# Kernel optimization log

Measured on AMD Instinct MI355X. Metric: run time of the kernel, lower is better.

Reference implementation:

```python
import jax, jax.numpy as jnp
import numpy as np

NUM_HEADS = 16


def setup_inputs() -> dict:
    key = jax.random.key(0)
    k1, k2, k3 = jax.random.split(key, 3)
    B, S, C = 1, 4096, 1024
    x = jax.random.normal(k1, (B, S, C), dtype=jnp.float32)
    # additive causal mask: 0 on/below diagonal, -1e9 above
    causal = jnp.triu(jnp.full((S, S), -1e9, dtype=jnp.float32), k=1)
    attention_mask = causal[None, None, :, :]
    W_attn = jax.random.normal(k2, (C, 3 * C), dtype=jnp.float32) * (C ** -0.5)
    b_attn = jnp.zeros((3 * C,), dtype=jnp.float32)
    W_proj = jax.random.normal(k3, (C, C), dtype=jnp.float32) * (C ** -0.5)
    b_proj = jnp.zeros((C,), dtype=jnp.float32)
    return {"x": x, "attention_mask": attention_mask, "W_attn": W_attn,
            "b_attn": b_attn, "W_proj": W_proj, "b_proj": b_proj}


def reference(x, attention_mask, W_attn, b_attn, W_proj, b_proj):
    B, S, C = x.shape
    H = NUM_HEADS
    hd = C // H
    qkv = x @ W_attn + b_attn                      # [B,S,3C]
    q, k, v = jnp.split(qkv, 3, axis=-1)
    # [B,S,C] -> [B,H,S,hd]
    q = q.reshape(B, S, H, hd).transpose(0, 2, 1, 3)
    k = k.reshape(B, S, H, hd).transpose(0, 2, 1, 3)
    v = v.reshape(B, S, H, hd).transpose(0, 2, 1, 3)
    att = jnp.einsum('bhqd,bhkd->bhqk', q, k) / jnp.sqrt(jnp.float32(hd))
    att = att + attention_mask                     # additive causal mask
    att = jax.nn.softmax(att, axis=-1)             # dropout is identity (p=0/eval)
    out = jnp.einsum('bhqk,bhkd->bhqd', att, v)    # [B,H,S,hd]
    out = out.transpose(0, 2, 1, 3).reshape(B, S, C)
    return out @ W_proj + b_proj
```

## Files before the change

kernel.cpp:

```cpp
#include <hip/hip_runtime.h>
#include <stdint.h>


typedef __bf16 bf16x8 __attribute__((ext_vector_type(8)));
typedef float f32x4 __attribute__((ext_vector_type(4)));

#define QSCALE 0.18033688011112042f

__device__ __forceinline__ f32x4 mfma16(bf16x8 a, bf16x8 b, f32x4 c) {
  return __builtin_amdgcn_mfma_f32_16x16x32_bf16(a, b, c, 0, 0, 0);
}

__device__ __forceinline__ void g2l16(const void* g, void* l) {
  __builtin_amdgcn_global_load_lds(
      (const __attribute__((address_space(1))) unsigned int*)g,
      (__attribute__((address_space(3))) unsigned int*)l,
      16, 0, 0);
}

__device__ __forceinline__ uint16_t f2bf(float f) {
  unsigned int u = __builtin_bit_cast(unsigned int, f);
  u += 0x7fffu + ((u >> 16) & 1u);
  return (uint16_t)(u >> 16);
}

__device__ __forceinline__ unsigned int pack_hi(float lo, float hi) {
  return __builtin_amdgcn_perm(__builtin_bit_cast(unsigned int, hi),
                               __builtin_bit_cast(unsigned int, lo), 0x07060302u);
}

__global__ __launch_bounds__(256) void f2b_k(const float* __restrict__ in,
                                             uint16_t* __restrict__ out, int n) {
  const int base = (blockIdx.x * 256 + threadIdx.x) * 8;
  if (base >= n) return;
  float4 a = *(const float4*)(in + base);
  float4 b = *(const float4*)(in + base + 4);
  uint16_t t[8];
  t[0] = f2bf(a.x); t[1] = f2bf(a.y); t[2] = f2bf(a.z); t[3] = f2bf(a.w);
  t[4] = f2bf(b.x); t[5] = f2bf(b.y); t[6] = f2bf(b.z); t[7] = f2bf(b.w);
  *(int4*)(out + base) = *(const int4*)t;
}

__global__ __launch_bounds__(256) void transpose2_f2b(const float* __restrict__ inA,
                                                      uint16_t* __restrict__ outA,
                                                      const float* __restrict__ inB,
                                                      uint16_t* __restrict__ outB) {
  __shared__ float t[64][65];
  const int tx = threadIdx.x & 15;
  const int ty = threadIdx.x >> 4;
  const bool isA = blockIdx.x < 48;
  const float* in = isA ? inA : inB;
  uint16_t* out = isA ? outA : outB;
  const int C = isA ? 3072 : 1024;
  const int bx = isA ? blockIdx.x : (blockIdx.x - 48);
  const int r0 = blockIdx.y * 64, c0 = bx * 64;
#pragma unroll
  for (int rr = ty; rr < 64; rr += 16) {
    float4 v = *(const float4*)(in + (size_t)(r0 + rr) * C + c0 + tx * 4);
    t[rr][tx * 4 + 0] = v.x; t[rr][tx * 4 + 1] = v.y;
    t[rr][tx * 4 + 2] = v.z; t[rr][tx * 4 + 3] = v.w;
  }
  __syncthreads();
#pragma unroll
  for (int cc = ty; cc < 64; cc += 16) {
    uint16_t tmp[4];
#pragma unroll
    for (int j = 0; j < 4; j++) tmp[j] = f2bf(t[tx * 4 + j][cc]);
    *(uint2*)(out + (size_t)(c0 + cc) * 1024 + r0 + tx * 4) = *(const uint2*)tmp;
  }
}

template <int EPI>
__global__ __launch_bounds__(256) void gemm_bt(const uint16_t* __restrict__ A,
                                               const uint16_t* __restrict__ Bt,
                                               const float* __restrict__ bias,
                                               uint16_t* __restrict__ outQ,
                                               uint16_t* __restrict__ outK,
                                               uint16_t* __restrict__ outV,
                                               float* __restrict__ outF) {
  __shared__ __align__(16) uint16_t lA[2][128 * 32];
  __shared__ __align__(16) uint16_t lB[2][128 * 32];
  const int tid = threadIdx.x;
  const int w = tid >> 6, lane = tid & 63;
  const int quad = lane >> 4, c16 = lane & 15;

  const int nwg = gridDim.x * gridDim.y;
  const int lin = blockIdx.y * gridDim.x + blockIdx.x;
  const int swz = (lin & 7) * (nwg >> 3) + (lin >> 3);
  const int m0 = (swz / gridDim.x) * 128, n0 = (swz % gridDim.x) * 128;

  f32x4 acc[4][4];
#pragma unroll
  for (int i = 0; i < 4; i++)
#pragma unroll
    for (int j = 0; j < 4; j++) acc[i][j] = f32x4{0.f, 0.f, 0.f, 0.f};

  const int instr = w * 2;
#define STAGE(BUF, K0)                                                          \
  _Pragma("unroll") for (int ii = 0; ii < 2; ii++) {                            \
    const int p16 = (instr + ii) * 64 + lane;                                   \
    const int row = p16 >> 2, cp = p16 & 3;                                     \
    const int c = cp ^ ((row >> 1) & 3);                                        \
    g2l16(A + (size_t)(m0 + row) * 1024 + (K0) + c * 8,                         \
          (char*)lA[BUF] + (size_t)(instr + ii) * 1024);                        \
    g2l16(Bt + (size_t)(n0 + row) * 1024 + (K0) + c * 8,                        \
          (char*)lB[BUF] + (size_t)(instr + ii) * 1024);                        \
  }

  STAGE(0, 0);
  asm volatile("s_waitcnt vmcnt(0)" ::: "memory");
  __syncthreads();

  int cur = 0;
  for (int k0 = 0; k0 < 1024; k0 += 32) {
    if (k0 + 32 < 1024) STAGE(cur ^ 1, k0 + 32);

    bf16x8 af[4], bfr[4];
#pragma unroll
    for (int t = 0; t < 4; t++) {
      const int mr = (w >> 1) * 64 + t * 16 + c16;
      af[t] = *(const bf16x8*)((const char*)lA[cur] + mr * 64 + ((quad ^ ((mr >> 1) & 3)) * 16));
      const int nr = (w & 1) * 64 + t * 16 + c16;
      bfr[t] = *(const bf16x8*)((const char*)lB[cur] + nr * 64 + ((quad ^ ((nr >> 1) & 3)) * 16));
    }
#pragma unroll
    for (int i = 0; i < 4; i++)
#pragma unroll
      for (int j = 0; j < 4; j++) acc[i][j] = mfma16(af[i], bfr[j], acc[i][j]);

    __syncthreads();
    cur ^= 1;
  }

  const int mbase = m0 + (w >> 1) * 64;
  const int nbase = n0 + (w & 1) * 64;
  float bv[4];
#pragma unroll
  for (int j = 0; j < 4; j++) bv[j] = bias[nbase + j * 16 + c16];
#pragma unroll
  for (int i = 0; i < 4; i++) {
#pragma unroll
    for (int j = 0; j < 4; j++) {
      const int n = nbase + j * 16 + c16;
#pragma unroll
      for (int r = 0; r < 4; r++) {
        const int m = mbase + i * 16 + quad * 4 + r;
        float fv = acc[i][j][r] + bv[j];
        if (EPI == 0) {
          const int region = n >> 10;
          const int cr = n & 1023;
          const int h = cr >> 6, d = cr & 63;
          if (region == 0)      outQ[((size_t)(h << 12) + m) * 64 + d] = f2bf(fv * QSCALE);
          else if (region == 1) outK[((size_t)(h << 12) + m) * 64 + d] = f2bf(fv);
          else                  outV[(((size_t)(h * 32 + (m >> 7)) * 64 + d) << 7) + (m & 127)] = f2bf(fv);
        } else {
          outF[(size_t)m * 1024 + n] = fv;
        }
      }
    }
  }
#undef STAGE
}

__global__ __launch_bounds__(256, 2) void attn_kernel(const uint16_t* __restrict__ Qb,
                                                      const uint16_t* __restrict__ Kb,
                                                      const uint16_t* __restrict__ Vtb,
                                                      uint16_t* __restrict__ Ob) {
  __shared__ __align__(16) uint16_t lX[4][2][64 * 64];
  __shared__ float lL[4][64];
  const int tid = threadIdx.x;
  const int w = tid >> 6;
  const int lane = tid & 63;
  const int quad = lane >> 4, c16 = lane & 15;
  const int c7 = c16 & 7;
  const int bid = blockIdx.x;
  const int h = bid & 15;
  const int sw = 63 - (bid >> 4);
  const int q0w = sw * 64;
  const int jmax = sw >> 1;

  const int stage_off = (lane >> 3) * 64 + (((lane & 7) ^ (lane >> 3)) << 3);

#define STAGE_K(BUF, KBH)                                                       \
  _Pragma("unroll") for (int s = 0; s < 8; s++)                                 \
      g2l16((KBH) + s * 512 + stage_off, (char*)lX[w][BUF] + s * 1024);

  bf16x8 qf[4][2];
#pragma unroll
  for (int ntq = 0; ntq < 4; ntq++)
#pragma unroll
    for (int kc = 0; kc < 2; kc++) {
      int4 v = *(const int4*)(Qb + ((size_t)(h << 12) + q0w + ntq * 16 + c16) * 64 + kc * 32 + quad * 8);
      qf[ntq][kc] = __builtin_bit_cast(bf16x8, v);
    }

  float ls[4] = {0.f, 0.f, 0.f, 0.f};
  f32x4 o[4][4];
#pragma unroll
  for (int i = 0; i < 4; i++)
#pragma unroll
    for (int nq = 0; nq < 4; nq++) o[i][nq] = f32x4{0.f, 0.f, 0.f, 0.f};

  {
    const uint16_t* kb0 = Kb + ((size_t)(h << 12) + w * 128) * 64;
    STAGE_K(0, kb0);
  }

  for (int j = w; j <= jmax; j += 4) {
    const uint16_t* kbase = Kb + ((size_t)(h << 12) + j * 128) * 64;
    const uint16_t* vbase = Vtb + (((size_t)(h * 32 + j) * 64) << 7);

#pragma unroll
    for (int half = 0; half < 2; half++) {
      if (half == 0) {
        STAGE_K(1, kbase + 4096);
        asm volatile("s_waitcnt vmcnt(8)" ::: "memory");
      } else if (j + 4 <= jmax) {
        const uint16_t* kbn = Kb + ((size_t)(h << 12) + (j + 4) * 128) * 64;
        STAGE_K(0, kbn);
        asm volatile("s_waitcnt vmcnt(8)" ::: "memory");
      } else {
        asm volatile("s_waitcnt vmcnt(0)" ::: "memory");
      }

      bf16x8 kfr[2][4];
      const char* kx = (const char*)lX[w][half] + c16 * 128;
#pragma unroll
      for (int kc = 0; kc < 2; kc++)
#pragma unroll
        for (int mt = 0; mt < 4; mt++)
          kfr[kc][mt] = *(const bf16x8*)(kx + mt * 2048 + (((kc * 4 + quad) ^ c7) << 4));

#pragma unroll
      for (int qp = 0; qp < 2; qp++) {
        f32x4 st[4][2];
#pragma unroll
        for (int mt = 0; mt < 4; mt++) {
          st[mt][0] = f32x4{0.f, 0.f, 0.f, 0.f};
          st[mt][1] = f32x4{0.f, 0.f, 0.f, 0.f};
        }
        __builtin_amdgcn_s_setprio(1);
#pragma unroll
        for (int kc = 0; kc < 2; kc++)
#pragma unroll
          for (int mt = 0; mt < 4; mt++) {
            st[mt][0] = mfma16(kfr[kc][mt], qf[qp * 2 + 0][kc], st[mt][0]);
            st[mt][1] = mfma16(kfr[kc][mt], qf[qp * 2 + 1][kc], st[mt][1]);
          }
        __builtin_amdgcn_s_setprio(0);

        if (j == jmax) {
#pragma unroll
          for (int nt = 0; nt < 2; nt++) {
            const int qg = q0w + qp * 32 + nt * 16 + c16;
#pragma unroll
            for (int mt = 0; mt < 4; mt++)
#pragma unroll
              for (int rr = 0; rr < 4; rr++) {
                const int key = j * 128 + half * 64 + mt * 16 + quad * 4 + rr;
                if (key > qg) st[mt][nt][rr] = -1.0e9f;
              }
          }
        }

#pragma unroll
        for (int nt = 0; nt < 2; nt++) {
          float sum0 = 0.f, sum1 = 0.f;
          const int prow = qp * 32 + nt * 16 + c16;
          const size_t pbase = (size_t)prow * 128;
#pragma unroll
          for (int mt = 0; mt < 4; mt++) {
            float p0 = __builtin_amdgcn_exp2f(st[mt][nt][0]);
            float p1 = __builtin_amdgcn_exp2f(st[mt][nt][1]);
            float p2 = __builtin_amdgcn_exp2f(st[mt][nt][2]);
            float p3 = __builtin_amdgcn_exp2f(st[mt][nt][3]);
            sum0 += p0 + p1;
            sum1 += p2 + p3;
            const unsigned int lo = pack_hi(p0, p1);
            const unsigned int hi = pack_hi(p2, p3);
            const int chunk = mt * 2 + (quad >> 1);
            uint2* dst = (uint2*)((char*)lX[w][half] + pbase +
                                  ((chunk ^ (prow & 7)) << 4) + (quad & 1) * 8);
            *dst = make_uint2(lo, hi);
          }
          float sum = sum0 + sum1;
          sum += __shfl_xor(sum, 16);
          sum += __shfl_xor(sum, 32);
          ls[qp * 2 + nt] += sum;
        }
      }

#pragma unroll
      for (int kc2 = 0; kc2 < 2; kc2++) {
        int4 vf[4];
#pragma unroll
        for (int mt = 0; mt < 4; mt++)
          vf[mt] = *(const int4*)(vbase + ((mt * 16 + c16) << 7) +
                                  (half * 8 + kc2 * 4 + quad) * 8);
        bf16x8 pb[4];
#pragma unroll
        for (int ntq = 0; ntq < 4; ntq++) {
          const int prow = ntq * 16 + c16;
          pb[ntq] = *(const bf16x8*)((const char*)lX[w][half] + (size_t)prow * 128 +
                                     (((kc2 * 4 + quad) ^ (prow & 7)) << 4));
        }
        __builtin_amdgcn_s_setprio(1);
#pragma unroll
        for (int mt = 0; mt < 4; mt++) {
          bf16x8 a = __builtin_bit_cast(bf16x8, vf[mt]);
#pragma unroll
          for (int ntq = 0; ntq < 4; ntq++)
            o[mt][ntq] = mfma16(a, pb[ntq], o[mt][ntq]);
        }
        __builtin_amdgcn_s_setprio(0);
      }
    }
  }

  asm volatile("s_waitcnt vmcnt(0)" ::: "memory");

  float* oL = (float*)lX[w];
#pragma unroll
  for (int mt = 0; mt < 4; mt++)
#pragma unroll
    for (int ntq = 0; ntq < 4; ntq++)
#pragma unroll
      for (int rr = 0; rr < 4; rr++)
        oL[(mt * 16 + quad * 4 + rr) * 64 + ntq * 16 + c16] = o[mt][ntq][rr];
  if (quad == 0) {
#pragma unroll
    for (int ntq = 0; ntq < 4; ntq++) lL[w][ntq * 16 + c16] = ls[ntq];
  }
  __syncthreads();

  const int q = tid & 63, dq = tid >> 6;
  const float lsum = lL[0][q] + lL[1][q] + lL[2][q] + lL[3][q];
  const float inv = 1.f / lsum;
  uint16_t t[16] __attribute__((aligned(16)));
#pragma unroll
  for (int i = 0; i < 16; i++) {
    const int d = dq * 16 + i;
    const int off = d * 64 + q;
    float s = ((const float*)lX[0])[off] + ((const float*)lX[1])[off] +
              ((const float*)lX[2])[off] + ((const float*)lX[3])[off];
    t[i] = f2bf(s * inv);
  }
  uint16_t* dst = Ob + (size_t)(q0w + q) * 1024 + h * 64 + dq * 16;
  *(int4*)dst = *(const int4*)t;
  *(int4*)(dst + 8) = *(const int4*)(t + 8);
#undef STAGE_K
}

extern "C" void kernel_launch(void* const* d_in, const int* in_sizes, int n_in,
                              void* d_out, int out_size, void* d_ws, size_t ws_size,
                              hipStream_t stream) {
  const float* x      = (const float*)d_in[0];
  const float* W_attn = (const float*)d_in[2];
  const float* b_attn = (const float*)d_in[3];
  const float* W_proj = (const float*)d_in[4];
  const float* b_proj = (const float*)d_in[5];
  float* out = (float*)d_out;

  char* ws = (char*)d_ws;
  uint16_t* Ob  = (uint16_t*)(ws);
  uint16_t* wtA = (uint16_t*)(ws + 8388608);
  uint16_t* wtP = (uint16_t*)(ws + 14680064);
  uint16_t* Qb  = (uint16_t*)(ws + 16777216);
  uint16_t* Kb  = (uint16_t*)(ws + 25165824);
  uint16_t* Vtb = (uint16_t*)(ws + 33554432);
  uint16_t* xb  = (uint16_t*)(ws + 41943040);

  f2b_k<<<2048, 256, 0, stream>>>(x, xb, 4096 * 1024);
  transpose2_f2b<<<dim3(64, 16), 256, 0, stream>>>(W_attn, wtA, W_proj, wtP);
  gemm_bt<0><<<dim3(24, 32), 256, 0, stream>>>(xb, wtA, b_attn, Qb, Kb, Vtb, nullptr);
  attn_kernel<<<dim3(1024), 256, 0, stream>>>(Qb, Kb, Vtb, Ob);
  gemm_bt<1><<<dim3(8, 32), 256, 0, stream>>>(Ob, wtP, b_proj, nullptr, nullptr, nullptr, out);
}
```

Before: 238.4 us.

## Shrink attention K/P tiles to 32 keys to halve LDS and skip masked chunks

The attention kernel now stages and processes K in 32-key chunks instead of 64-key halves. This halves the per-wave LDS buffer so more blocks can be resident per CU. On the diagonal block it stops at the last chunk that contains unmasked keys, skipping fully masked work. The final cross-wave reduction of the output is split into two rounds so it fits the smaller LDS, at the cost of an extra barrier and more loop iterations with less MFMA work per wait.

```diff
diff --git a/kernel.cpp b/kernel.cpp
--- a/kernel.cpp
+++ b/kernel.cpp
@@ -166,7 +166,7 @@
                                                       const uint16_t* __restrict__ Kb,
                                                       const uint16_t* __restrict__ Vtb,
                                                       uint16_t* __restrict__ Ob) {
-  __shared__ __align__(16) uint16_t lX[4][2][64 * 64];
+  __shared__ __align__(16) uint16_t lX[4][2][32 * 64];
   __shared__ float lL[4][64];
   const int tid = threadIdx.x;
   const int w = tid >> 6;
@@ -181,8 +181,8 @@
 
   const int stage_off = (lane >> 3) * 64 + (((lane & 7) ^ (lane >> 3)) << 3);
 
-#define STAGE_K(BUF, KBH)                                                       \
-  _Pragma("unroll") for (int s = 0; s < 8; s++)                                 \
+#define STAGE32(BUF, KBH)                                                       \
+  _Pragma("unroll") for (int s = 0; s < 4; s++)                                 \
       g2l16((KBH) + s * 512 + stage_off, (char*)lX[w][BUF] + s * 1024);
 
   bf16x8 qf[4][2];
@@ -203,39 +203,40 @@
 
   {
     const uint16_t* kb0 = Kb + ((size_t)(h << 12) + w * 128) * 64;
-    STAGE_K(0, kb0);
-  }
-
+    STAGE32(0, kb0);
+  }
+
+  int par = 0;
   for (int j = w; j <= jmax; j += 4) {
     const uint16_t* kbase = Kb + ((size_t)(h << 12) + j * 128) * 64;
     const uint16_t* vbase = Vtb + (((size_t)(h * 32 + j) * 64) << 7);
-
-#pragma unroll
-    for (int half = 0; half < 2; half++) {
-      if (half == 0) {
-        STAGE_K(1, kbase + 4096);
-        asm volatile("s_waitcnt vmcnt(8)" ::: "memory");
+    const int chmax = (j == jmax) ? ((q0w + 63 - (j << 7)) >> 5) : 3;
+
+    for (int ch = 0; ch <= chmax; ++ch) {
+      if (ch < chmax) {
+        STAGE32(par ^ 1, kbase + (ch + 1) * 2048);
+        asm volatile("s_waitcnt vmcnt(4)" ::: "memory");
       } else if (j + 4 <= jmax) {
         const uint16_t* kbn = Kb + ((size_t)(h << 12) + (j + 4) * 128) * 64;
-        STAGE_K(0, kbn);
-        asm volatile("s_waitcnt vmcnt(8)" ::: "memory");
+        STAGE32(par ^ 1, kbn);
+        asm volatile("s_waitcnt vmcnt(4)" ::: "memory");
       } else {
         asm volatile("s_waitcnt vmcnt(0)" ::: "memory");
       }
 
-      bf16x8 kfr[2][4];
-      const char* kx = (const char*)lX[w][half] + c16 * 128;
+      bf16x8 kfr[2][2];
+      const char* kx = (const char*)lX[w][par] + c16 * 128;
 #pragma unroll
       for (int kc = 0; kc < 2; kc++)
 #pragma unroll
-        for (int mt = 0; mt < 4; mt++)
+        for (int mt = 0; mt < 2; mt++)
           kfr[kc][mt] = *(const bf16x8*)(kx + mt * 2048 + (((kc * 4 + quad) ^ c7) << 4));
 
 #pragma unroll
       for (int qp = 0; qp < 2; qp++) {
-        f32x4 st[4][2];
-#pragma unroll
-        for (int mt = 0; mt < 4; mt++) {
+        f32x4 st[2][2];
+#pragma unroll
+        for (int mt = 0; mt < 2; mt++) {
           st[mt][0] = f32x4{0.f, 0.f, 0.f, 0.f};
           st[mt][1] = f32x4{0.f, 0.f, 0.f, 0.f};
         }
@@ -243,7 +244,7 @@
 #pragma unroll
         for (int kc = 0; kc < 2; kc++)
 #pragma unroll
-          for (int mt = 0; mt < 4; mt++) {
+          for (int mt = 0; mt < 2; mt++) {
             st[mt][0] = mfma16(kfr[kc][mt], qf[qp * 2 + 0][kc], st[mt][0]);
             st[mt][1] = mfma16(kfr[kc][mt], qf[qp * 2 + 1][kc], st[mt][1]);
           }
@@ -254,10 +255,10 @@
           for (int nt = 0; nt < 2; nt++) {
             const int qg = q0w + qp * 32 + nt * 16 + c16;
 #pragma unroll
-            for (int mt = 0; mt < 4; mt++)
+            for (int mt = 0; mt < 2; mt++)
 #pragma unroll
               for (int rr = 0; rr < 4; rr++) {
-                const int key = j * 128 + half * 64 + mt * 16 + quad * 4 + rr;
+                const int key = (j << 7) + ch * 32 + mt * 16 + quad * 4 + rr;
                 if (key > qg) st[mt][nt][rr] = -1.0e9f;
               }
           }
@@ -267,9 +268,9 @@
         for (int nt = 0; nt < 2; nt++) {
           float sum0 = 0.f, sum1 = 0.f;
           const int prow = qp * 32 + nt * 16 + c16;
-          const size_t pbase = (size_t)prow * 128;
-#pragma unroll
-          for (int mt = 0; mt < 4; mt++) {
+          const size_t pbase = (size_t)prow * 64;
+#pragma unroll
+          for (int mt = 0; mt < 2; mt++) {
             float p0 = __builtin_amdgcn_exp2f(st[mt][nt][0]);
             float p1 = __builtin_amdgcn_exp2f(st[mt][nt][1]);
             float p2 = __builtin_amdgcn_exp2f(st[mt][nt][2]);
@@ -278,9 +279,9 @@
             sum1 += p2 + p3;
             const unsigned int lo = pack_hi(p0, p1);
             const unsigned int hi = pack_hi(p2, p3);
-            const int chunk = mt * 2 + (quad >> 1);
-            uint2* dst = (uint2*)((char*)lX[w][half] + pbase +
-                                  ((chunk ^ (prow & 7)) << 4) + (quad & 1) * 8);
+            const int chunkc = mt * 2 + (quad >> 1);
+            uint2* dst = (uint2*)((char*)lX[w][par] + pbase +
+                                  ((chunkc ^ (prow & 3)) << 4) + (quad & 1) * 8);
             *dst = make_uint2(lo, hi);
           }
           float sum = sum0 + sum1;
@@ -290,65 +291,69 @@
         }
       }
 
-#pragma unroll
-      for (int kc2 = 0; kc2 < 2; kc2++) {
-        int4 vf[4];
-#pragma unroll
-        for (int mt = 0; mt < 4; mt++)
-          vf[mt] = *(const int4*)(vbase + ((mt * 16 + c16) << 7) +
-                                  (half * 8 + kc2 * 4 + quad) * 8);
-        bf16x8 pb[4];
-#pragma unroll
-        for (int ntq = 0; ntq < 4; ntq++) {
-          const int prow = ntq * 16 + c16;
-          pb[ntq] = *(const bf16x8*)((const char*)lX[w][half] + (size_t)prow * 128 +
-                                     (((kc2 * 4 + quad) ^ (prow & 7)) << 4));
-        }
-        __builtin_amdgcn_s_setprio(1);
-#pragma unroll
-        for (int mt = 0; mt < 4; mt++) {
-          bf16x8 a = __builtin_bit_cast(bf16x8, vf[mt]);
-#pragma unroll
-          for (int ntq = 0; ntq < 4; ntq++)
-            o[mt][ntq] = mfma16(a, pb[ntq], o[mt][ntq]);
-        }
-        __builtin_amdgcn_s_setprio(0);
-      }
+      int4 vf[4];
+#pragma unroll
+      for (int mt = 0; mt < 4; mt++)
+        vf[mt] = *(const int4*)(vbase + ((mt * 16 + c16) << 7) + ch * 32 + quad * 8);
+      bf16x8 pb[4];
+#pragma unroll
+      for (int ntq = 0; ntq < 4; ntq++) {
+        const int prow = ntq * 16 + c16;
+        pb[ntq] = *(const bf16x8*)((const char*)lX[w][par] + (size_t)prow * 64 +
+                                   (((quad) ^ (prow & 3)) << 4));
+      }
+      __builtin_amdgcn_s_setprio(1);
+#pragma unroll
+      for (int mt = 0; mt < 4; mt++) {
+        bf16x8 a = __builtin_bit_cast(bf16x8, vf[mt]);
+#pragma unroll
+        for (int ntq = 0; ntq < 4; ntq++)
+          o[mt][ntq] = mfma16(a, pb[ntq], o[mt][ntq]);
+      }
+      __builtin_amdgcn_s_setprio(0);
+
+      par ^= 1;
     }
   }
 
   asm volatile("s_waitcnt vmcnt(0)" ::: "memory");
 
-  float* oL = (float*)lX[w];
-#pragma unroll
-  for (int mt = 0; mt < 4; mt++)
-#pragma unroll
-    for (int ntq = 0; ntq < 4; ntq++)
-#pragma unroll
-      for (int rr = 0; rr < 4; rr++)
-        oL[(mt * 16 + quad * 4 + rr) * 64 + ntq * 16 + c16] = o[mt][ntq][rr];
   if (quad == 0) {
 #pragma unroll
     for (int ntq = 0; ntq < 4; ntq++) lL[w][ntq * 16 + c16] = ls[ntq];
   }
-  __syncthreads();
 
   const int q = tid & 63, dq = tid >> 6;
-  const float lsum = lL[0][q] + lL[1][q] + lL[2][q] + lL[3][q];
-  const float inv = 1.f / lsum;
-  uint16_t t[16] __attribute__((aligned(16)));
-#pragma unroll
-  for (int i = 0; i < 16; i++) {
-    const int d = dq * 16 + i;
-    const int off = d * 64 + q;
-    float s = ((const float*)lX[0])[off] + ((const float*)lX[1])[off] +
-              ((const float*)lX[2])[off] + ((const float*)lX[3])[off];
-    t[i] = f2bf(s * inv);
-  }
-  uint16_t* dst = Ob + (size_t)(q0w + q) * 1024 + h * 64 + dq * 16;
-  *(int4*)dst = *(const int4*)t;
-  *(int4*)(dst + 8) = *(const int4*)(t + 8);
-#undef STAGE_K
+  float inv = 0.f;
+#pragma unroll
+  for (int round = 0; round < 2; ++round) {
+    float* oL = (float*)lX[w];
+#pragma unroll
+    for (int mt = 0; mt < 2; mt++)
+#pragma unroll
+      for (int ntq = 0; ntq < 4; ntq++)
+#pragma unroll
+        for (int rr = 0; rr < 4; rr++)
+          oL[(mt * 16 + quad * 4 + rr) * 64 + ntq * 16 + c16] =
+              o[round * 2 + mt][ntq][rr];
+    __syncthreads();
+    if (round == 0) {
+      const float lsum = lL[0][q] + lL[1][q] + lL[2][q] + lL[3][q];
+      inv = 1.f / lsum;
+    }
+    uint16_t t[8] __attribute__((aligned(16)));
+#pragma unroll
+    for (int i = 0; i < 8; i++) {
+      const int off = (dq * 8 + i) * 64 + q;
+      float s = ((const float*)lX[0])[off] + ((const float*)lX[1])[off] +
+                ((const float*)lX[2])[off] + ((const float*)lX[3])[off];
+      t[i] = f2bf(s * inv);
+    }
+    *(int4*)(Ob + (size_t)(q0w + q) * 1024 + h * 64 + round * 32 + dq * 8) =
+        *(const int4*)t;
+    if (round == 0) __syncthreads();
+  }
+#undef STAGE32
 }
 
 extern "C" void kernel_launch(void* const* d_in, const int* in_sizes, int n_in,
```

After: 244.8 us. 1.03x slower.
